# Kernel optimization log

Measured on AMD Instinct MI355X. Metric: run time of the kernel, lower is better.

Reference implementation:

```python
import jax, jax.numpy as jnp
import numpy as np

B, N, C = 16, 1024, 256
SIZE = (512, 640)          # (H, W) image size
STRIDE = 8
H0, W0 = SIZE[0] // STRIDE, SIZE[1] // STRIDE   # 64, 80
P_TOK = H0 * W0                                  # 5120 base tokens
NHEAD, NLVL, NPTS = 8, 4, 4
HD = C // NHEAD
NUM_CLASSES = 7


def setup_inputs() -> dict:
    key = jax.random.key(0)
    ks = jax.random.split(key, 16)
    g = lambda k, shape, s=0.02: jax.random.normal(k, shape, jnp.float32) * s
    return {
        "q_t": jax.random.normal(ks[0], (B, N, C), jnp.float32),
        "h_t": jax.random.normal(ks[1], (B, P_TOK, C), jnp.float32),
        "p_head_t": jax.random.uniform(ks[2], (B, N, 2), jnp.float32)
                    * jnp.array([SIZE[1], SIZE[0]], jnp.float32),  # (x,y) in image coords
        "W_off": g(ks[3], (C, NHEAD * NLVL * NPTS * 2)),
        "b_off": g(ks[4], (NHEAD * NLVL * NPTS * 2,)),
        "W_attn": g(ks[5], (C, NHEAD * NLVL * NPTS)),
        "b_attn": g(ks[6], (NHEAD * NLVL * NPTS,)),
        "W_v": g(ks[7], (C, C)), "b_v": g(ks[8], (C,)),
        "W_o": g(ks[9], (C, C)), "b_o": g(ks[10], (C,)),
        "W_p1": g(ks[11], (2 * C, C)), "b_p1": g(ks[12], (C,)),
        "W_p2": g(ks[13], (C, NUM_CLASSES)), "b_p2": g(ks[14], (NUM_CLASSES,)),
    }


def _bilinear_sample(value_l, loc):
    """value_l: (B,Hl,Wl,nh,hd); loc: (B,N,nh,NPTS,2) in [0,1] normalized (x,y).
    grid_sample semantics: align_corners=False, padding_mode='zeros'.
    Returns (B,nh,N,NPTS,hd)."""
    Bb, Hl, Wl = value_l.shape[0], value_l.shape[1], value_l.shape[2]
    x = loc[..., 0] * Wl - 0.5
    y = loc[..., 1] * Hl - 0.5
    x0 = jnp.floor(x); y0 = jnp.floor(y)
    wx = x - x0; wy = y - y0
    x0i = x0.astype(jnp.int32); y0i = y0.astype(jnp.int32)
    flat = value_l.reshape(Bb, Hl * Wl, NHEAD, HD).transpose(0, 2, 1, 3)  # (B,nh,S,hd)

    def corner(xi, yi):
        valid = ((xi >= 0) & (xi < Wl) & (yi >= 0) & (yi < Hl)).astype(value_l.dtype)
        idx = (jnp.clip(yi, 0, Hl - 1) * Wl + jnp.clip(xi, 0, Wl - 1)).transpose(0, 2, 1, 3)  # (B,nh,N,P)
        g = jnp.take_along_axis(flat, idx.reshape(Bb, NHEAD, -1)[..., None], axis=2)
        g = g.reshape(Bb, NHEAD, idx.shape[2], idx.shape[3], HD)
        return g * valid.transpose(0, 2, 1, 3)[..., None]

    tw = lambda w: w.transpose(0, 2, 1, 3)[..., None]  # (B,nh,N,P,1)
    return (corner(x0i, y0i) * tw((1 - wx) * (1 - wy))
            + corner(x0i + 1, y0i) * tw(wx * (1 - wy))
            + corner(x0i, y0i + 1) * tw((1 - wx) * wy)
            + corner(x0i + 1, y0i + 1) * tw(wx * wy))


def reference(q_t, h_t, p_head_t, W_off, b_off, W_attn, b_attn,
              W_v, b_v, W_o, b_o, W_p1, b_p1, W_p2, b_p2):
    # normalize point predictions to [0,1] (x by W, y by H)
    p_norm = jnp.clip(p_head_t / jnp.array([SIZE[1], SIZE[0]], jnp.float32), 0.0, 1.0)

    # ---- get_deformable_inputs: 4-level pyramid by 2x2 average pooling ----
    cur = h_t.reshape(B, H0, W0, C)
    feats, shapes = [], []
    for l in range(NLVL):
        feats.append(cur)
        shapes.append((cur.shape[1], cur.shape[2]))
        if l < NLVL - 1:
            h, w = cur.shape[1], cur.shape[2]
            cur = cur.reshape(B, h // 2, 2, w // 2, 2, C).mean(axis=(2, 4))
    f_scales = jnp.concatenate([f.reshape(B, -1, C) for f in feats], axis=1)  # (B,S,C)

    # ---- DMSMHA_Block (multi-scale deformable attention) ----
    value = (f_scales @ W_v + b_v).reshape(B, -1, NHEAD, HD)
    offsets = (q_t @ W_off + b_off).reshape(B, N, NHEAD, NLVL, NPTS, 2)
    attn = jax.nn.softmax(
        (q_t @ W_attn + b_attn).reshape(B, N, NHEAD, NLVL * NPTS), axis=-1
    ).reshape(B, N, NHEAD, NLVL, NPTS)

    out = jnp.zeros((B, NHEAD, N, HD), jnp.float32)
    start = 0
    for l, (Hl, Wl) in enumerate(shapes):
        Sl = Hl * Wl
        vl = value[:, start:start + Sl].reshape(B, Hl, Wl, NHEAD, HD)
        start += Sl
        norm = jnp.array([Wl, Hl], jnp.float32)
        loc = p_norm[:, :, None, None, :] + offsets[:, :, :, l] / norm  # (B,N,nh,P,2)
        sampled = _bilinear_sample(vl, loc)                              # (B,nh,N,P,hd)
        w = attn[:, :, :, l].transpose(0, 2, 1, 3)                       # (B,nh,N,P)
        out = out + jnp.einsum('bhnp,bhnpd->bhnd', w, sampled)

    q_local = out.transpose(0, 2, 1, 3).reshape(B, N, C) @ W_o + b_o

    # ---- fuse + MLP head ----
    q_fused = jnp.concatenate([q_t, q_local], axis=-1)
    hid = jax.nn.relu(q_fused @ W_p1 + b_p1)
    logits = hid @ W_p2 + b_p2   # (B,N,num_classes)
    return logits
```

## Files before the change

### kernel.cpp

```cpp
#include <hip/hip_runtime.h>
#include <math.h>


namespace {

constexpr int kB = 16;
constexpr int kN = 1024;
constexpr int kC = 256;
constexpr int kNCLS = 7;
constexpr int kSTOT = 6800;

typedef __attribute__((ext_vector_type(8))) short short8;
typedef __attribute__((ext_vector_type(4))) float f32x4;

__device__ inline ushort f2bf(float f) {
  union { float f; unsigned u; } v; v.f = f;
  unsigned r = (v.u + 0x7fffu + ((v.u >> 16) & 1u)) >> 16;
  return (ushort)r;
}
__device__ inline float bf2f(ushort h) {
  union { unsigned u; float f; } v; v.u = ((unsigned)h) << 16;
  return v.f;
}

__device__ inline void gload16(const ushort* g, ushort* l) {
  __builtin_amdgcn_global_load_lds(
      (const __attribute__((address_space(1))) void*)g,
      (__attribute__((address_space(3))) void*)l, 16, 0, 0);
}

__global__ void cast_f2b_kernel(const float* __restrict__ in, ushort* __restrict__ out, int n4) {
  int i = blockIdx.x * 256 + threadIdx.x;
  if (i >= n4) return;
  float4 v = ((const float4*)in)[i];
  ((ushort4*)out)[i] = make_ushort4(f2bf(v.x), f2bf(v.y), f2bf(v.z), f2bf(v.w));
}

__global__ void pool_all_kernel(ushort* __restrict__ val) {
  int blk = blockIdx.x;
  int X = blk % 10;
  int t2 = blk / 10;
  int Y = t2 % 8;
  int b = t2 / 8;
  int c = threadIdx.x;
  const ushort* base = val + (((size_t)b * kSTOT + (Y * 8) * 80 + X * 8) << 8) + c;

  float l1[16];
#pragma unroll
  for (int i = 0; i < 16; ++i) {
    int iy = i >> 2, ix = i & 3;
    const ushort* p = base + (((iy * 2) * 80 + ix * 2) << 8);
    l1[i] = 0.25f * (bf2f(p[0]) + bf2f(p[256]) + bf2f(p[80 * 256]) + bf2f(p[80 * 256 + 256]));
  }
#pragma unroll
  for (int i = 0; i < 16; ++i) {
    int iy = i >> 2, ix = i & 3;
    val[(((size_t)b * kSTOT + 5120 + (Y * 4 + iy) * 40 + X * 4 + ix) << 8) + c] = f2bf(l1[i]);
  }
  float l2[4];
#pragma unroll
  for (int j = 0; j < 4; ++j) {
    int jy = j >> 1, jx = j & 1;
    l2[j] = 0.25f * (l1[(2 * jy) * 4 + 2 * jx] + l1[(2 * jy) * 4 + 2 * jx + 1] +
                     l1[(2 * jy + 1) * 4 + 2 * jx] + l1[(2 * jy + 1) * 4 + 2 * jx + 1]);
    val[(((size_t)b * kSTOT + 6400 + (Y * 2 + jy) * 20 + X * 2 + jx) << 8) + c] = f2bf(l2[j]);
  }
  float l3 = 0.25f * (l2[0] + l2[1] + l2[2] + l2[3]);
  val[(((size_t)b * kSTOT + 6720 + Y * 10 + X) << 8) + c] = f2bf(l3);
}

__global__ void wtrans_all_kernel(const float* __restrict__ s0, const float* __restrict__ s1,
                                  const float* __restrict__ s2, const float* __restrict__ s3,
                                  const float* __restrict__ s4,
                                  ushort* __restrict__ d0, ushort* __restrict__ d1,
                                  ushort* __restrict__ d2, ushort* __restrict__ d3,
                                  ushort* __restrict__ d4) {
  __shared__ float t[32][33];
  const float* W; ushort* Wt; int K, N;
  switch (blockIdx.z) {
    case 0: W = s0; Wt = d0; K = 256; N = 256; break;
    case 1: W = s1; Wt = d1; K = 256; N = 256; break;
    case 2: W = s2; Wt = d2; K = 256; N = 128; break;
    case 3: W = s3; Wt = d3; K = 256; N = 256; break;
    default: W = s4; Wt = d4; K = 512; N = 256; break;
  }
  int nx = blockIdx.x << 5, ky = blockIdx.y << 5;
  if (nx >= N || ky >= K) return;
  int lx = threadIdx.x & 31, ly = threadIdx.x >> 5;
#pragma unroll
  for (int i = 0; i < 32; i += 8)
    t[ly + i][lx] = W[(size_t)(ky + ly + i) * N + nx + lx];
  __syncthreads();
#pragma unroll
  for (int i = 0; i < 32; i += 8)
    Wt[(size_t)(nx + ly + i) * K + ky + lx] = f2bf(t[lx][ly + i]);
}

__global__ void wcomb_kernel(const float* __restrict__ W_o, const float* __restrict__ W_p1,
                             const float* __restrict__ b_o, const float* __restrict__ b_p1,
                             const ushort* __restrict__ Wt_p1,
                             ushort* __restrict__ Wt_p1c, float* __restrict__ bp1c) {
  __shared__ float wcol[256];
  __shared__ float wsum[4];
  int h = blockIdx.x;
  int in = threadIdx.x;
  wcol[in] = W_p1[(size_t)(256 + in) * 256 + h];
  __syncthreads();
  float s = 0.f;
  const float* wo = W_o + (size_t)in * 256;
#pragma unroll 4
  for (int out = 0; out < 256; ++out) s = fmaf(wo[out], wcol[out], s);
  Wt_p1c[(size_t)h * 512 + 256 + in] = f2bf(s);
  Wt_p1c[(size_t)h * 512 + in] = Wt_p1[(size_t)h * 512 + in];
  float part = b_o[in] * wcol[in];
#pragma unroll
  for (int m = 32; m > 0; m >>= 1) part += __shfl_xor(part, m);
  if ((in & 63) == 0) wsum[in >> 6] = part;
  __syncthreads();
  if (in == 0) bp1c[h] = b_p1[h] + wsum[0] + wsum[1] + wsum[2] + wsum[3];
}

template <int KTOT, bool SPLITK, int OMODE, bool RELU>
__global__ __launch_bounds__(256) void gemm_bf16_kernel(
    const ushort* __restrict__ A, const ushort* __restrict__ A2,
    const ushort* __restrict__ Wt, const float* __restrict__ bias,
    const float* __restrict__ bias2, void* __restrict__ Cout,
    void* __restrict__ Cout2, int ldc) {
  __shared__ ushort Asm[2][128 * 32];
  __shared__ ushort Bsm[2][128 * 32];
  const int tid = threadIdx.x;
  const int w = tid >> 6, l = tid & 63;
  const int bm = blockIdx.y << 7, bn = blockIdx.x << 7;
  const int wm = w >> 1, wn = w & 1;

  const int c0 = w * 2, c1 = w * 2 + 1;
  const int G0 = c0 * 64 + l, G1 = c1 * 64 + l;
  const int r0 = G0 >> 2, g0 = G0 & 3;
  const int r1 = G1 >> 2, g1 = G1 & 3;
  const int sz0 = (g0 ^ ((r0 >> 1) & 3)) << 3;
  const int sz1 = (g1 ^ ((r1 >> 1) & 3)) << 3;
  const int ak = SPLITK ? 256 : KTOT;
  const ushort* sA0 = A + (size_t)(bm + r0) * ak + sz0;
  const ushort* sA1 = A + (size_t)(bm + r1) * ak + sz1;
  const ushort* sA0b = SPLITK ? A2 + (size_t)(bm + r0) * 256 + sz0 : nullptr;
  const ushort* sA1b = SPLITK ? A2 + (size_t)(bm + r1) * 256 + sz1 : nullptr;
  const ushort* sB0 = Wt + (size_t)(bn + r0) * KTOT + sz0;
  const ushort* sB1 = Wt + (size_t)(bn + r1) * KTOT + sz1;

  const int e = l >> 4, rl = l & 15;
  int aoff[4], boff[4];
#pragma unroll
  for (int i = 0; i < 4; ++i) {
    int r = wm * 64 + i * 16 + rl;
    aoff[i] = r * 32 + ((e ^ ((r >> 1) & 3)) << 3);
    int rb = wn * 64 + i * 16 + rl;
    boff[i] = rb * 32 + ((e ^ ((rb >> 1) & 3)) << 3);
  }

  f32x4 acc[4][4];
#pragma unroll
  for (int i = 0; i < 4; ++i)
#pragma unroll
    for (int j = 0; j < 4; ++j) acc[i][j] = (f32x4){0.f, 0.f, 0.f, 0.f};

  auto stage = [&](int buf, int k0) {
    const ushort *a0, *a1;
    if (SPLITK && k0 >= 256) {
      a0 = sA0b + (k0 - 256);
      a1 = sA1b + (k0 - 256);
    } else {
      a0 = sA0 + k0;
      a1 = sA1 + k0;
    }
    gload16(a0, &Asm[buf][c0 * 512]);
    gload16(a1, &Asm[buf][c1 * 512]);
    gload16(sB0 + k0, &Bsm[buf][c0 * 512]);
    gload16(sB1 + k0, &Bsm[buf][c1 * 512]);
  };

  constexpr int nt = KTOT / 32;
  stage(0, 0);
  __syncthreads();
  for (int t = 0; t < nt; ++t) {
    const int cur = t & 1;
    if (t + 1 < nt) stage(cur ^ 1, (t + 1) * 32);
    short8 af[4], bfr[4];
#pragma unroll
    for (int i = 0; i < 4; ++i) af[i] = *(const short8*)&Asm[cur][aoff[i]];
#pragma unroll
    for (int j = 0; j < 4; ++j) bfr[j] = *(const short8*)&Bsm[cur][boff[j]];
#pragma unroll
    for (int i = 0; i < 4; ++i)
#pragma unroll
      for (int j = 0; j < 4; ++j)
        acc[i][j] = __builtin_amdgcn_mfma_f32_16x16x32_bf16(bfr[j], af[i], acc[i][j], 0, 0, 0);
    __syncthreads();
  }

#pragma unroll
  for (int j = 0; j < 4; ++j) {
    int ch = bn + wn * 64 + j * 16 + e * 4;
    float4 b4;
    if (OMODE == 2)
      b4 = (ch < 256) ? *(const float4*)(bias + ch) : *(const float4*)(bias2 + ch - 256);
    else
      b4 = *(const float4*)(bias + ch);
    float bv[4] = {b4.x, b4.y, b4.z, b4.w};
#pragma unroll
    for (int i = 0; i < 4; ++i) {
      int sp = bm + wm * 64 + i * 16 + rl;
      float v[4];
#pragma unroll
      for (int r = 0; r < 4; ++r) {
        v[r] = acc[i][j][r] + bv[r];
        if (RELU) v[r] = fmaxf(v[r], 0.f);
      }
      if (OMODE == 0) {
        *(float4*)&((float*)Cout)[(size_t)sp * ldc + ch] = make_float4(v[0], v[1], v[2], v[3]);
      } else if (OMODE == 1) {
        *(ushort4*)&((ushort*)Cout)[(size_t)sp * ldc + ch] =
            make_ushort4(f2bf(v[0]), f2bf(v[1]), f2bf(v[2]), f2bf(v[3]));
      } else {
        if (ch < 256)
          *(float4*)&((float*)Cout)[(size_t)sp * 256 + ch] = make_float4(v[0], v[1], v[2], v[3]);
        else
          *(float4*)&((float*)Cout2)[(size_t)sp * 128 + (ch - 256)] =
              make_float4(v[0], v[1], v[2], v[3]);
      }
    }
  }
}

__global__ __launch_bounds__(256) void gemm_f32a_kernel(
    const float* __restrict__ A, const ushort* __restrict__ Wt,
    const float* __restrict__ bias, ushort* __restrict__ Cout) {
  __shared__ ushort Asm[128 * 32];
  __shared__ ushort Bsm[128 * 32];
  const int tid = threadIdx.x;
  const int w = tid >> 6, l = tid & 63;
  const int by = blockIdx.y;
  const int bn = blockIdx.x << 7;
  const int bm = by << 7;
  const int wm = w >> 1, wn = w & 1;

  const int ar = tid >> 1, ah = tid & 1;
  const float* aSrc = A + (size_t)(bm + ar) * 256 + ah * 16;
  const int s_ar = (ar >> 1) & 3;
  const int ad0 = ar * 32 + (((2 * ah + 0) ^ s_ar) << 3);
  const int ad1 = ar * 32 + (((2 * ah + 1) ^ s_ar) << 3);

  const int c0 = w * 2, c1 = w * 2 + 1;
  const int G0 = c0 * 64 + l, G1 = c1 * 64 + l;
  const int r0 = G0 >> 2, g0 = G0 & 3;
  const int r1 = G1 >> 2, g1 = G1 & 3;
  const ushort* sB0 = Wt + (size_t)(bn + r0) * 256 + ((g0 ^ ((r0 >> 1) & 3)) << 3);
  const ushort* sB1 = Wt + (size_t)(bn + r1) * 256 + ((g1 ^ ((r1 >> 1) & 3)) << 3);

  const int e = l >> 4, rl = l & 15;
  int aoff[4], boff[4];
#pragma unroll
  for (int i = 0; i < 4; ++i) {
    int r = wm * 64 + i * 16 + rl;
    aoff[i] = r * 32 + ((e ^ ((r >> 1) & 3)) << 3);
    int rb = wn * 64 + i * 16 + rl;
    boff[i] = rb * 32 + ((e ^ ((rb >> 1) & 3)) << 3);
  }

  f32x4 acc[4][4];
#pragma unroll
  for (int i = 0; i < 4; ++i)
#pragma unroll
    for (int j = 0; j < 4; ++j) acc[i][j] = (f32x4){0.f, 0.f, 0.f, 0.f};

  float4 av[4];
  auto loadA = [&](int k0) {
#pragma unroll
    for (int q = 0; q < 4; ++q) av[q] = *(const float4*)(aSrc + k0 + 4 * q);
  };
  auto writeA = [&]() {
    ushort u[16];
#pragma unroll
    for (int q = 0; q < 4; ++q) {
      u[4 * q + 0] = f2bf(av[q].x);
      u[4 * q + 1] = f2bf(av[q].y);
      u[4 * q + 2] = f2bf(av[q].z);
      u[4 * q + 3] = f2bf(av[q].w);
    }
    *(short8*)&Asm[ad0] = (short8){(short)u[0], (short)u[1], (short)u[2], (short)u[3],
                                   (short)u[4], (short)u[5], (short)u[6], (short)u[7]};
    *(short8*)&Asm[ad1] = (short8){(short)u[8], (short)u[9], (short)u[10], (short)u[11],
                                   (short)u[12], (short)u[13], (short)u[14], (short)u[15]};
  };
  auto stageB = [&](int k0) {
    gload16(sB0 + k0, &Bsm[c0 * 512]);
    gload16(sB1 + k0, &Bsm[c1 * 512]);
  };

  loadA(0);
  for (int t = 0; t < 8; ++t) {
    if (t) __syncthreads();
    writeA();
    stageB(t * 32);
    __syncthreads();
    short8 af[4], bfr[4];
#pragma unroll
    for (int i = 0; i < 4; ++i) af[i] = *(const short8*)&Asm[aoff[i]];
#pragma unroll
    for (int j = 0; j < 4; ++j) bfr[j] = *(const short8*)&Bsm[boff[j]];
    if (t < 7) loadA((t + 1) * 32);
#pragma unroll
    for (int i = 0; i < 4; ++i)
#pragma unroll
      for (int j = 0; j < 4; ++j)
        acc[i][j] = __builtin_amdgcn_mfma_f32_16x16x32_bf16(bfr[j], af[i], acc[i][j], 0, 0, 0);
  }

  const int b = by / 40;
  const int sb = (by - b * 40) << 7;
  ushort* outB = Cout + (((size_t)(b * 6800 + sb)) << 8);
#pragma unroll
  for (int j = 0; j < 4; ++j) {
    int ch = bn + wn * 64 + j * 16 + e * 4;
    float4 b4 = *(const float4*)(bias + ch);
    float bv[4] = {b4.x, b4.y, b4.z, b4.w};
#pragma unroll
    for (int i = 0; i < 4; ++i) {
      int sp = wm * 64 + i * 16 + rl;
      float v[4];
#pragma unroll
      for (int r = 0; r < 4; ++r) v[r] = acc[i][j][r] + bv[r];
      *(ushort4*)&outB[(size_t)sp * 256 + ch] =
          make_ushort4(f2bf(v[0]), f2bf(v[1]), f2bf(v[2]), f2bf(v[3]));
    }
  }
}

__global__ void deform_kernel(
    const ushort* __restrict__ value, const float* __restrict__ off,
    const float* __restrict__ attnl, const float* __restrict__ p_head,
    ushort* __restrict__ samp) {
  int blk = (int)blockIdx.x;
  int sw = (blk & 7) * 256 + (blk >> 3);
  int wvi = (sw << 2) + (threadIdx.x >> 6);
  int l = threadIdx.x & 63;
  int nq = l >> 5;
  int lh = l & 31;
  int h = lh >> 2;
  int pt = wvi * 2 + nq;
  int b = pt >> 10;
  size_t bn = (size_t)pt;

  float ph = (lh < 2) ? p_head[bn * 2 + lh] : 0.f;
  float px = __shfl(ph, (nq << 5) + 0, 64) * (1.0f / 640.0f);
  float py = __shfl(ph, (nq << 5) + 1, 64) * (1.0f / 512.0f);
  px = fminf(fmaxf(px, 0.f), 1.f);
  py = fminf(fmaxf(py, 0.f), 1.f);

  const float4* offp = (const float4*)(off + (bn << 8));
  float4 ofv0 = offp[2 * lh];
  float4 ofv1 = offp[2 * lh + 1];
  float4 atv = ((const float4*)(attnl + (bn << 7)))[lh];

  float m = fmaxf(fmaxf(atv.x, atv.y), fmaxf(atv.z, atv.w));
  m = fmaxf(m, __shfl_xor(m, 1, 64));
  m = fmaxf(m, __shfl_xor(m, 2, 64));
  float e0 = expf(atv.x - m), e1 = expf(atv.y - m);
  float e2 = expf(atv.z - m), e3 = expf(atv.w - m);
  float s = e0 + e1 + e2 + e3;
  s += __shfl_xor(s, 1, 64);
  s += __shfl_xor(s, 2, 64);
  float inv = 1.f / s;
  atv = make_float4(e0 * inv, e1 * inv, e2 * inv, e3 * inv);

  float acc[8];
#pragma unroll
  for (int i = 0; i < 8; ++i) acc[i] = 0.f;
  const ushort* vbb = value + (((size_t)b * kSTOT) << 8) + (lh << 3);

#pragma unroll 1
  for (int lv = 0; lv < 4; ++lv) {
    const int Wl = 80 >> lv, Hl = 64 >> lv;
    const int offL = (lv == 0) ? 0 : (lv == 1) ? 5120 : (lv == 2) ? 6400 : 6720;
    const ushort* vb = vbb + (((size_t)offL) << 8);
    const int src = (nq << 5) + (h << 2) + lv;
    const float fx = px * (float)Wl - 0.5f;
    const float fy = py * (float)Hl - 0.5f;
#pragma unroll
    for (int pp = 0; pp < 4; ++pp) {
      float sx, sy;
      if ((pp >> 1) == 0) {
        sx = (pp & 1) ? ofv0.z : ofv0.x;
        sy = (pp & 1) ? ofv0.w : ofv0.y;
      } else {
        sx = (pp & 1) ? ofv1.z : ofv1.x;
        sy = (pp & 1) ? ofv1.w : ofv1.y;
      }
      float ox = __shfl(sx, src, 64);
      float oy = __shfl(sy, src, 64);
      float sa = pp == 0 ? atv.x : pp == 1 ? atv.y : pp == 2 ? atv.z : atv.w;
      float aw = __shfl(sa, src, 64);

      float xx = fx + ox;
      float yy = fy + oy;
      float x0f = floorf(xx), y0f = floorf(yy);
      float wx = xx - x0f, wy = yy - y0f;
      int x0 = (int)x0f, y0 = (int)y0f;
      float w00 = (1.f - wx) * (1.f - wy) * aw;
      float w01 = wx * (1.f - wy) * aw;
      float w10 = (1.f - wx) * wy * aw;
      float w11 = wx * wy * aw;
      auto corner = [&](int xi, int yi, float wgt) {
        bool valid = (xi >= 0) && (xi < Wl) && (yi >= 0) && (yi < Hl);
        int xc = xi < 0 ? 0 : (xi > Wl - 1 ? Wl - 1 : xi);
        int yc = yi < 0 ? 0 : (yi > Hl - 1 ? Hl - 1 : yi);
        short8 d = *(const short8*)(vb + (((size_t)(yc * Wl + xc)) << 8));
        float wg = valid ? wgt : 0.f;
#pragma unroll
        for (int i = 0; i < 8; ++i) acc[i] = fmaf(wg, bf2f((ushort)d[i]), acc[i]);
      };
      corner(x0, y0, w00);
      corner(x0 + 1, y0, w01);
      corner(x0, y0 + 1, w10);
      corner(x0 + 1, y0 + 1, w11);
    }
  }
  ushort o[8];
#pragma unroll
  for (int i = 0; i < 8; ++i) o[i] = f2bf(acc[i]);
  *(short8*)(samp + (bn << 8) + (lh << 3)) =
      (short8){(short)o[0], (short)o[1], (short)o[2], (short)o[3],
               (short)o[4], (short)o[5], (short)o[6], (short)o[7]};
}

__global__ void head_kernel(const float* __restrict__ hid, const float* __restrict__ W2,
                            const float* __restrict__ b2, float* __restrict__ outp) {
  int gid = blockIdx.x * 256 + threadIdx.x;
  int wave = gid >> 6;
  int lane = threadIdx.x & 63;
  if (wave >= kB * kN) return;
  const float* hrow = hid + ((size_t)wave << 8);
  float acc[kNCLS];
#pragma unroll
  for (int j = 0; j < kNCLS; ++j) acc[j] = 0.f;
  for (int k = lane; k < kC; k += 64) {
    float hv = hrow[k];
    const float* wr = W2 + k * kNCLS;
#pragma unroll
    for (int j = 0; j < kNCLS; ++j) acc[j] = fmaf(hv, wr[j], acc[j]);
  }
#pragma unroll
  for (int m = 32; m > 0; m >>= 1) {
#pragma unroll
    for (int j = 0; j < kNCLS; ++j) acc[j] += __shfl_xor(acc[j], m);
  }
  float r = 0.f;
#pragma unroll
  for (int j = 0; j < kNCLS; ++j)
    if (lane == j) r = acc[j] + b2[j];
  if (lane < kNCLS) outp[(size_t)wave * kNCLS + lane] = r;
}

}

extern "C" void kernel_launch(void* const* d_in, const int* in_sizes, int n_in,
                              void* d_out, int out_size, void* d_ws, size_t ws_size,
                              hipStream_t stream) {
  const float* q_t    = (const float*)d_in[0];
  const float* h_t    = (const float*)d_in[1];
  const float* p_head = (const float*)d_in[2];
  const float* W_off  = (const float*)d_in[3];
  const float* b_off  = (const float*)d_in[4];
  const float* W_attn = (const float*)d_in[5];
  const float* b_attn = (const float*)d_in[6];
  const float* W_v    = (const float*)d_in[7];
  const float* b_v    = (const float*)d_in[8];
  const float* W_o    = (const float*)d_in[9];
  const float* b_o    = (const float*)d_in[10];
  const float* W_p1   = (const float*)d_in[11];
  const float* b_p1   = (const float*)d_in[12];
  const float* W_p2   = (const float*)d_in[13];
  const float* b_p2   = (const float*)d_in[14];
  float* out = (float*)d_out;
  char* wsb = (char*)d_ws;

  ushort* value = (ushort*)(wsb + 55705600);
  ushort* q_bf  = (ushort*)(wsb + 111411200);
  float*  offb  = (float*)(wsb + 119799808);
  float*  attnl = (float*)(wsb + 136577024);
  ushort* samp  = (ushort*)(wsb + 144965632);
  float*  hid   = (float*)(wsb + 161742848);
  ushort* wtp   = (ushort*)(wsb + 178520064);
  ushort* Wt_v   = wtp;
  ushort* Wt_oa  = wtp + 65536;
  ushort* Wt_o   = wtp + 163840;
  ushort* Wt_p1  = wtp + 229376;
  ushort* Wt_p1c = wtp + 360448;
  float*  bp1c   = (float*)(wtp + 491520);

  cast_f2b_kernel<<<4096, 256, 0, stream>>>(q_t, q_bf, kB * kN * 64);

  wtrans_all_kernel<<<dim3(8, 16, 5), 256, 0, stream>>>(
      W_v, W_off, W_attn, W_o, W_p1,
      Wt_v, Wt_oa, Wt_oa + 65536, Wt_o, Wt_p1);

  wcomb_kernel<<<256, 256, 0, stream>>>(W_o, W_p1, b_o, b_p1, Wt_p1, Wt_p1c, bp1c);

  gemm_f32a_kernel<<<dim3(2, 640), 256, 0, stream>>>(h_t, Wt_v, b_v, value);

  pool_all_kernel<<<1280, 256, 0, stream>>>(value);

  gemm_bf16_kernel<256, false, 2, false><<<dim3(3, 128), 256, 0, stream>>>(
      q_bf, nullptr, Wt_oa, b_off, b_attn, offb, attnl, 256);

  deform_kernel<<<2048, 256, 0, stream>>>(value, offb, attnl, p_head, samp);

  gemm_bf16_kernel<512, true, 0, true><<<dim3(2, 128), 256, 0, stream>>>(
      q_bf, samp, Wt_p1c, bp1c, nullptr, hid, nullptr, 256);

  head_kernel<<<4096, 256, 0, stream>>>(hid, W_p2, b_p2, out);
}
```

Measured before the change: 144.7 us.

## Double-buffer value-projection GEMM and halve its M tile to 64

The fp32-input value projection GEMM now uses 64-row M tiles instead of 128, which doubles the grid to 2x1280 blocks. Its A and B shared-memory tiles are double-buffered so the next K-slice's global loads and bf16 conversion overlap the current MFMAs, with one barrier per iteration. The aim is more blocks for occupancy and better latency hiding on a memory-bound GEMM. In exchange the B (weight) tile is reloaded twice as often and each block does less MFMA work.

```diff
diff --git a/kernel.cpp b/kernel.cpp
--- a/kernel.cpp
+++ b/kernel.cpp
@@ -234,20 +234,18 @@
 __global__ __launch_bounds__(256) void gemm_f32a_kernel(
     const float* __restrict__ A, const ushort* __restrict__ Wt,
     const float* __restrict__ bias, ushort* __restrict__ Cout) {
-  __shared__ ushort Asm[128 * 32];
-  __shared__ ushort Bsm[128 * 32];
+  __shared__ ushort Asm[2][64 * 32];
+  __shared__ ushort Bsm[2][128 * 32];
   const int tid = threadIdx.x;
   const int w = tid >> 6, l = tid & 63;
   const int by = blockIdx.y;
   const int bn = blockIdx.x << 7;
-  const int bm = by << 7;
+  const int bm = by << 6;
   const int wm = w >> 1, wn = w & 1;
 
-  const int ar = tid >> 1, ah = tid & 1;
-  const float* aSrc = A + (size_t)(bm + ar) * 256 + ah * 16;
-  const int s_ar = (ar >> 1) & 3;
-  const int ad0 = ar * 32 + (((2 * ah + 0) ^ s_ar) << 3);
-  const int ad1 = ar * 32 + (((2 * ah + 1) ^ s_ar) << 3);
+  const int ar = tid >> 2, aq = tid & 3;
+  const float* aSrc = A + (size_t)(bm + ar) * 256 + aq * 8;
+  const int adst = ar * 32 + ((aq ^ ((ar >> 1) & 3)) << 3);
 
   const int c0 = w * 2, c1 = w * 2 + 1;
   const int G0 = c0 * 64 + l, G1 = c1 * 64 + l;
@@ -257,66 +255,65 @@
   const ushort* sB1 = Wt + (size_t)(bn + r1) * 256 + ((g1 ^ ((r1 >> 1) & 3)) << 3);
 
   const int e = l >> 4, rl = l & 15;
-  int aoff[4], boff[4];
-#pragma unroll
-  for (int i = 0; i < 4; ++i) {
-    int r = wm * 64 + i * 16 + rl;
+  int aoff[2], boff[4];
+#pragma unroll
+  for (int i = 0; i < 2; ++i) {
+    int r = wm * 32 + i * 16 + rl;
     aoff[i] = r * 32 + ((e ^ ((r >> 1) & 3)) << 3);
-    int rb = wn * 64 + i * 16 + rl;
-    boff[i] = rb * 32 + ((e ^ ((rb >> 1) & 3)) << 3);
-  }
-
-  f32x4 acc[4][4];
-#pragma unroll
-  for (int i = 0; i < 4; ++i)
+  }
+#pragma unroll
+  for (int j = 0; j < 4; ++j) {
+    int rb = wn * 64 + j * 16 + rl;
+    boff[j] = rb * 32 + ((e ^ ((rb >> 1) & 3)) << 3);
+  }
+
+  f32x4 acc[2][4];
+#pragma unroll
+  for (int i = 0; i < 2; ++i)
 #pragma unroll
     for (int j = 0; j < 4; ++j) acc[i][j] = (f32x4){0.f, 0.f, 0.f, 0.f};
 
-  float4 av[4];
+  float4 av0, av1;
   auto loadA = [&](int k0) {
-#pragma unroll
-    for (int q = 0; q < 4; ++q) av[q] = *(const float4*)(aSrc + k0 + 4 * q);
+    av0 = *(const float4*)(aSrc + k0);
+    av1 = *(const float4*)(aSrc + k0 + 4);
   };
-  auto writeA = [&]() {
-    ushort u[16];
-#pragma unroll
-    for (int q = 0; q < 4; ++q) {
-      u[4 * q + 0] = f2bf(av[q].x);
-      u[4 * q + 1] = f2bf(av[q].y);
-      u[4 * q + 2] = f2bf(av[q].z);
-      u[4 * q + 3] = f2bf(av[q].w);
+  auto writeA = [&](int buf) {
+    *(short8*)&Asm[buf][adst] =
+        (short8){(short)f2bf(av0.x), (short)f2bf(av0.y), (short)f2bf(av0.z), (short)f2bf(av0.w),
+                 (short)f2bf(av1.x), (short)f2bf(av1.y), (short)f2bf(av1.z), (short)f2bf(av1.w)};
+  };
+  auto stageB = [&](int buf, int k0) {
+    gload16(sB0 + k0, &Bsm[buf][c0 * 512]);
+    gload16(sB1 + k0, &Bsm[buf][c1 * 512]);
+  };
+
+  loadA(0);
+  stageB(0, 0);
+  writeA(0);
+  __syncthreads();
+  for (int t = 0; t < 8; ++t) {
+    const int cur = t & 1;
+    if (t < 7) {
+      loadA((t + 1) * 32);
+      stageB(cur ^ 1, (t + 1) * 32);
     }
-    *(short8*)&Asm[ad0] = (short8){(short)u[0], (short)u[1], (short)u[2], (short)u[3],
-                                   (short)u[4], (short)u[5], (short)u[6], (short)u[7]};
-    *(short8*)&Asm[ad1] = (short8){(short)u[8], (short)u[9], (short)u[10], (short)u[11],
-                                   (short)u[12], (short)u[13], (short)u[14], (short)u[15]};
-  };
-  auto stageB = [&](int k0) {
-    gload16(sB0 + k0, &Bsm[c0 * 512]);
-    gload16(sB1 + k0, &Bsm[c1 * 512]);
-  };
-
-  loadA(0);
-  for (int t = 0; t < 8; ++t) {
-    if (t) __syncthreads();
-    writeA();
-    stageB(t * 32);
-    __syncthreads();
-    short8 af[4], bfr[4];
-#pragma unroll
-    for (int i = 0; i < 4; ++i) af[i] = *(const short8*)&Asm[aoff[i]];
-#pragma unroll
-    for (int j = 0; j < 4; ++j) bfr[j] = *(const short8*)&Bsm[boff[j]];
-    if (t < 7) loadA((t + 1) * 32);
-#pragma unroll
-    for (int i = 0; i < 4; ++i)
+    short8 af[2], bfr[4];
+#pragma unroll
+    for (int i = 0; i < 2; ++i) af[i] = *(const short8*)&Asm[cur][aoff[i]];
+#pragma unroll
+    for (int j = 0; j < 4; ++j) bfr[j] = *(const short8*)&Bsm[cur][boff[j]];
+#pragma unroll
+    for (int i = 0; i < 2; ++i)
 #pragma unroll
       for (int j = 0; j < 4; ++j)
         acc[i][j] = __builtin_amdgcn_mfma_f32_16x16x32_bf16(bfr[j], af[i], acc[i][j], 0, 0, 0);
-  }
-
-  const int b = by / 40;
-  const int sb = (by - b * 40) << 7;
+    if (t < 7) writeA(cur ^ 1);
+    __syncthreads();
+  }
+
+  const int b = by / 80;
+  const int sb = (by - b * 80) << 6;
   ushort* outB = Cout + (((size_t)(b * 6800 + sb)) << 8);
 #pragma unroll
   for (int j = 0; j < 4; ++j) {
@@ -324,8 +321,8 @@
     float4 b4 = *(const float4*)(bias + ch);
     float bv[4] = {b4.x, b4.y, b4.z, b4.w};
 #pragma unroll
-    for (int i = 0; i < 4; ++i) {
-      int sp = wm * 64 + i * 16 + rl;
+    for (int i = 0; i < 2; ++i) {
+      int sp = wm * 32 + i * 16 + rl;
       float v[4];
 #pragma unroll
       for (int r = 0; r < 4; ++r) v[r] = acc[i][j][r] + bv[r];
@@ -505,7 +502,7 @@
 
   wcomb_kernel<<<256, 256, 0, stream>>>(W_o, W_p1, b_o, b_p1, Wt_p1, Wt_p1c, bp1c);
 
-  gemm_f32a_kernel<<<dim3(2, 640), 256, 0, stream>>>(h_t, Wt_v, b_v, value);
+  gemm_f32a_kernel<<<dim3(2, 1280), 256, 0, stream>>>(h_t, Wt_v, b_v, value);
 
   pool_all_kernel<<<1280, 256, 0, stream>>>(value);
 
```

After: 145.0 us. Within noise of the previous version (+0.2%).
